# Kernel optimization log

Measured on AMD Instinct MI355X. Metric: run time of the kernel, lower is better.

Reference implementation:

```python
import jax, jax.numpy as jnp
import numpy as np

EC = 32
N = 500000
DIV_EPS = 1e-8
NO_PENALTY_THRESH = 0.005

def _rotation_matrices(rpy):
    # rpy: [EC,3] roll-pitch-yaw -> [EC,3,3]
    c = jnp.cos(rpy); s = jnp.sin(rpy)
    cx, cy, cz = c[:, 0], c[:, 1], c[:, 2]
    sx, sy, sz = s[:, 0], s[:, 1], s[:, 2]
    R = jnp.stack([
        cz * cy, cz * sy * sx - sz * cx, cz * sy * cx + sz * sx,
        sz * cy, sz * sy * sx + cz * cx, sz * sy * cx - cz * sx,
        -sy,     cy * sx,                cy * cx,
    ], axis=-1)
    return R.reshape(rpy.shape[:-1] + (3, 3))

def _eval_rbf(samples, centers, radii, rotations):
    # samples [N,3], centers/radii/rotations [EC,3] -> [EC,N]
    d = 1.0 / (radii + DIV_EPS)                      # inverse diag covariances
    R = _rotation_matrices(rotations)                # [EC,3,3]
    inv_cov = jnp.einsum('eij,ej,ekj->eik', R, d, R) # R diag(d) R^T, symmetric
    diff = samples[None, :, :] - centers[:, None, :] # [EC,N,3]
    quad = jnp.einsum('eni,eij,enj->en', diff, inv_cov, diff)
    return jnp.exp(-0.5 * quad)

def setup_inputs() -> dict:
    key = jax.random.key(0)
    ks = jax.random.split(key, 7)
    u = lambda k, shape, lo, hi: jax.random.uniform(k, shape, jnp.float32, lo, hi)
    return {
        'world_space_points': jax.random.normal(ks[0], (N, 3), jnp.float32),
        'nerflet_activations': jax.random.normal(ks[1], (EC, N, 4), jnp.float32),
        'dists': jax.random.uniform(ks[2], (N, 1), jnp.float32),
        'constants': u(ks[3], (EC, 1), 10.0, 20.0),
        'centers': u(ks[4], (EC, 3), -0.45, 0.45),
        'radii': u(ks[5], (EC, 1), 0.05, 0.06),
        'rotations': u(ks[6], (EC, 3), -np.pi, np.pi),
    }

def reference(world_space_points, nerflet_activations, dists, constants, centers, radii, rotations):
    c = jnp.abs(constants)                            # [EC,1]
    r3 = jnp.tile(jnp.abs(radii), (1, 3))             # [EC,3]
    rbfs = _eval_rbf(world_space_points, centers, r3, rotations)[:, :, None]  # [EC,N,1]
    rbfs = rbfs * c[:, None, :]                       # scaled by |constants|
    penalty = jnp.mean(jnp.sum(jnp.abs(rbfs - NO_PENALTY_THRESH), axis=0))
    alpha = 1.0 - jnp.exp(-jax.nn.relu(nerflet_activations[..., -1:]) * dists[None])  # [EC,N,1]
    rgb = jax.nn.sigmoid(nerflet_activations[..., :3])
    na = jnp.concatenate([rgb, alpha], axis=-1)       # [EC,N,4]
    rbf_sums = jnp.sum(rbfs, axis=0, keepdims=True)   # [1,N,1]
    rbfs_norm = rbfs / (rbf_sums + 0.01)
    outputs = jnp.sum(na * rbfs_norm, axis=0)         # [N,4]
    return outputs, penalty
```

## Files before the change

kernel.cpp:

```cpp
#include <hip/hip_runtime.h>
#include <math.h>

#define EC 32
#define BLOCK 256

typedef float fvec4 __attribute__((ext_vector_type(4)));

__global__ __launch_bounds__(BLOCK) void ldif_main_kernel(
    const float* __restrict__ pts,
    const fvec4* __restrict__ act,
    const float* __restrict__ dists,
    const float* __restrict__ constants,
    const float* __restrict__ centers,
    const float* __restrict__ radii,
    const float* __restrict__ rotations,
    fvec4* __restrict__ out,
    float* __restrict__ partials,
    int n) {
    __shared__ float4 sp[EC * 3];
    __shared__ float red[BLOCK];
    int tid = threadIdx.x;
    if (tid < EC) {
        int e = tid;
        float r = fabsf(radii[e]);
        float dinv = 1.0f / (r + 1e-8f);
        float rx = rotations[3 * e + 0], ry = rotations[3 * e + 1], rz = rotations[3 * e + 2];
        float cx = cosf(rx), cy = cosf(ry), cz = cosf(rz);
        float sx = sinf(rx), sy = sinf(ry), sz = sinf(rz);
        float R00 = cz * cy, R01 = cz * sy * sx - sz * cx, R02 = cz * sy * cx + sz * sx;
        float R10 = sz * cy, R11 = sz * sy * sx + cz * cx, R12 = sz * sy * cx - cz * sx;
        float R20 = -sy,     R21 = cy * sx,                R22 = cy * cx;
        float ic00 = dinv * (R00 * R00 + R01 * R01 + R02 * R02);
        float ic11 = dinv * (R10 * R10 + R11 * R11 + R12 * R12);
        float ic22 = dinv * (R20 * R20 + R21 * R21 + R22 * R22);
        float ic01 = dinv * (R00 * R10 + R01 * R11 + R02 * R12);
        float ic02 = dinv * (R00 * R20 + R01 * R21 + R02 * R22);
        float ic12 = dinv * (R10 * R20 + R11 * R21 + R12 * R22);
        const float NH = -0.72134752044f;
        float lc = log2f(fabsf(constants[e]));
        sp[3 * e + 0] = make_float4(centers[3 * e + 0], centers[3 * e + 1], centers[3 * e + 2], lc);
        sp[3 * e + 1] = make_float4(NH * ic00, NH * ic11, NH * ic22, 2.0f * NH * ic01);
        sp[3 * e + 2] = make_float4(2.0f * NH * ic02, 2.0f * NH * ic12, 0.0f, 0.0f);
    }
    __syncthreads();

    long long i = (long long)blockIdx.x * BLOCK + tid;
    float pen = 0.0f;
    if (i < n) {
        float px = pts[3 * i + 0];
        float py = pts[3 * i + 1];
        float pz = pts[3 * i + 2];
        float dl = dists[i] * 1.44269504f;

        float s = 0.0f;
        float a0 = 0.0f, a1 = 0.0f, a2 = 0.0f, a3 = 0.0f;
#pragma unroll 8
        for (int e = 0; e < EC; ++e) {
            fvec4 a = __builtin_nontemporal_load(&act[(size_t)e * (size_t)n + (size_t)i]);
            float4 p0 = sp[3 * e + 0];
            float4 p1 = sp[3 * e + 1];
            float4 p2 = sp[3 * e + 2];
            float dx = px - p0.x, dy = py - p0.y, dz = pz - p0.z;
            float q = (p1.x * dx + p1.w * dy + p2.x * dz) * dx
                    + (p1.y * dy + p2.y * dz) * dy
                    + (p1.z * dz) * dz
                    + p0.w;
            float v = __builtin_amdgcn_exp2f(q);
            s += v;
            pen += fabsf(v - 0.005f);
            float s0 = __builtin_amdgcn_rcpf(1.0f + __builtin_amdgcn_exp2f(-1.44269504f * a.x));
            float s1 = __builtin_amdgcn_rcpf(1.0f + __builtin_amdgcn_exp2f(-1.44269504f * a.y));
            float s2 = __builtin_amdgcn_rcpf(1.0f + __builtin_amdgcn_exp2f(-1.44269504f * a.z));
            float al = 1.0f - __builtin_amdgcn_exp2f(-fmaxf(a.w, 0.0f) * dl);
            a0 += v * s0;
            a1 += v * s1;
            a2 += v * s2;
            a3 += v * al;
        }
        float rn = __builtin_amdgcn_rcpf(s + 0.01f);
        fvec4 o;
        o.x = a0 * rn; o.y = a1 * rn; o.z = a2 * rn; o.w = a3 * rn;
        __builtin_nontemporal_store(o, &out[i]);
    }

    red[tid] = pen;
    __syncthreads();
    for (int st = BLOCK / 2; st > 0; st >>= 1) {
        if (tid < st) red[tid] += red[tid + st];
        __syncthreads();
    }
    if (tid == 0) partials[blockIdx.x] = red[0];
}

__global__ __launch_bounds__(BLOCK) void ldif_reduce_kernel(
    const float* __restrict__ partials, int nparts, float* __restrict__ out, int n) {
    __shared__ double rd[BLOCK];
    int tid = threadIdx.x;
    double s = 0.0;
    for (int j = tid; j < nparts; j += BLOCK) s += (double)partials[j];
    rd[tid] = s;
    __syncthreads();
    for (int st = BLOCK / 2; st > 0; st >>= 1) {
        if (tid < st) rd[tid] += rd[tid + st];
        __syncthreads();
    }
    if (tid == 0) out[0] = (float)(rd[0] / (double)n);
}

extern "C" void kernel_launch(void* const* d_in, const int* in_sizes, int n_in,
                              void* d_out, int out_size, void* d_ws, size_t ws_size,
                              hipStream_t stream) {
    const float* pts       = (const float*)d_in[0];
    const float* act       = (const float*)d_in[1];
    const float* dists     = (const float*)d_in[2];
    const float* constants = (const float*)d_in[3];
    const float* centers   = (const float*)d_in[4];
    const float* radii     = (const float*)d_in[5];
    const float* rotations = (const float*)d_in[6];
    float* out = (float*)d_out;

    int n = in_sizes[0] / 3;
    float* partials = (float*)d_ws;

    int nblocks = (n + BLOCK - 1) / BLOCK;

    ldif_main_kernel<<<nblocks, BLOCK, 0, stream>>>(
        pts, (const fvec4*)act, dists, constants, centers, radii, rotations,
        (fvec4*)out, partials, n);
    ldif_reduce_kernel<<<1, BLOCK, 0, stream>>>(partials, nblocks, out + (size_t)4 * n, n);
}
```

Before: 51.13 us.

## Fuse penalty reduction via last-block atomic counter and process two points per thread

Removes the separate reduce kernel launch by having the last block to finish, detected through an atomic counter zeroed by a memset, perform the final penalty sum. Each thread now handles two points, which gives it more independent loads and exp work in flight and halves the number of blocks. The block reduction switches to wavefront shuffles. In exchange it adds a memset and the atomic/fence logic, and raises register pressure.

```diff
diff --git a/kernel.cpp b/kernel.cpp
--- a/kernel.cpp
+++ b/kernel.cpp
@@ -3,10 +3,11 @@
 
 #define EC 32
 #define BLOCK 256
+#define PPT 2
 
 typedef float fvec4 __attribute__((ext_vector_type(4)));
 
-__global__ __launch_bounds__(BLOCK) void ldif_main_kernel(
+__global__ __launch_bounds__(BLOCK) void ldif_fused_kernel(
     const float* __restrict__ pts,
     const fvec4* __restrict__ act,
     const float* __restrict__ dists,
@@ -15,11 +16,16 @@
     const float* __restrict__ radii,
     const float* __restrict__ rotations,
     fvec4* __restrict__ out,
+    float* __restrict__ penout,
     float* __restrict__ partials,
-    int n) {
+    unsigned int* __restrict__ counter,
+    int n, int nblocks) {
     __shared__ float4 sp[EC * 3];
-    __shared__ float red[BLOCK];
-    int tid = threadIdx.x;
+    __shared__ float sred[4];
+    __shared__ double rd[BLOCK];
+    __shared__ int sdone;
+
+    const int tid = threadIdx.x;
     if (tid < EC) {
         int e = tid;
         float r = fabsf(radii[e]);
@@ -44,67 +50,101 @@
     }
     __syncthreads();
 
-    long long i = (long long)blockIdx.x * BLOCK + tid;
+    const long long i0 = (long long)blockIdx.x * (BLOCK * PPT) + tid;
+    const long long i1 = i0 + BLOCK;
+    const bool v1 = (i1 < n);
+    const long long iq = v1 ? i1 : i0;
+
     float pen = 0.0f;
-    if (i < n) {
-        float px = pts[3 * i + 0];
-        float py = pts[3 * i + 1];
-        float pz = pts[3 * i + 2];
-        float dl = dists[i] * 1.44269504f;
+    {
+        const float LOG2E = 1.44269504f;
+        float pxp = __builtin_nontemporal_load(&pts[3 * i0 + 0]);
+        float pyp = __builtin_nontemporal_load(&pts[3 * i0 + 1]);
+        float pzp = __builtin_nontemporal_load(&pts[3 * i0 + 2]);
+        float dlp = __builtin_nontemporal_load(&dists[i0]) * LOG2E;
+        float pxq = __builtin_nontemporal_load(&pts[3 * iq + 0]);
+        float pyq = __builtin_nontemporal_load(&pts[3 * iq + 1]);
+        float pzq = __builtin_nontemporal_load(&pts[3 * iq + 2]);
+        float dlq = __builtin_nontemporal_load(&dists[iq]) * LOG2E;
 
-        float s = 0.0f;
-        float a0 = 0.0f, a1 = 0.0f, a2 = 0.0f, a3 = 0.0f;
-#pragma unroll 8
+        float sP = 0.f, p0P = 0.f, p1P = 0.f, p2P = 0.f, p3P = 0.f, penP = 0.f;
+        float sQ = 0.f, p0Q = 0.f, p1Q = 0.f, p2Q = 0.f, p3Q = 0.f, penQ = 0.f;
+#pragma unroll 4
         for (int e = 0; e < EC; ++e) {
-            fvec4 a = __builtin_nontemporal_load(&act[(size_t)e * (size_t)n + (size_t)i]);
-            float4 p0 = sp[3 * e + 0];
-            float4 p1 = sp[3 * e + 1];
-            float4 p2 = sp[3 * e + 2];
-            float dx = px - p0.x, dy = py - p0.y, dz = pz - p0.z;
-            float q = (p1.x * dx + p1.w * dy + p2.x * dz) * dx
-                    + (p1.y * dy + p2.y * dz) * dy
-                    + (p1.z * dz) * dz
-                    + p0.w;
-            float v = __builtin_amdgcn_exp2f(q);
-            s += v;
-            pen += fabsf(v - 0.005f);
-            float s0 = __builtin_amdgcn_rcpf(1.0f + __builtin_amdgcn_exp2f(-1.44269504f * a.x));
-            float s1 = __builtin_amdgcn_rcpf(1.0f + __builtin_amdgcn_exp2f(-1.44269504f * a.y));
-            float s2 = __builtin_amdgcn_rcpf(1.0f + __builtin_amdgcn_exp2f(-1.44269504f * a.z));
-            float al = 1.0f - __builtin_amdgcn_exp2f(-fmaxf(a.w, 0.0f) * dl);
-            a0 += v * s0;
-            a1 += v * s1;
-            a2 += v * s2;
-            a3 += v * al;
+            fvec4 ap = __builtin_nontemporal_load(&act[(size_t)e * (size_t)n + (size_t)i0]);
+            fvec4 aq = __builtin_nontemporal_load(&act[(size_t)e * (size_t)n + (size_t)iq]);
+            float4 c0 = sp[3 * e + 0];
+            float4 c1 = sp[3 * e + 1];
+            float4 c2 = sp[3 * e + 2];
+            {
+                float dx = pxp - c0.x, dy = pyp - c0.y, dz = pzp - c0.z;
+                float q = (c1.x * dx + c1.w * dy + c2.x * dz) * dx
+                        + (c1.y * dy + c2.y * dz) * dy
+                        + (c1.z * dz) * dz + c0.w;
+                float v = __builtin_amdgcn_exp2f(q);
+                sP += v;
+                penP += fabsf(v - 0.005f);
+                float s0 = __builtin_amdgcn_rcpf(1.0f + __builtin_amdgcn_exp2f(-LOG2E * ap.x));
+                float s1 = __builtin_amdgcn_rcpf(1.0f + __builtin_amdgcn_exp2f(-LOG2E * ap.y));
+                float s2 = __builtin_amdgcn_rcpf(1.0f + __builtin_amdgcn_exp2f(-LOG2E * ap.z));
+                float al = 1.0f - __builtin_amdgcn_exp2f(-fmaxf(ap.w, 0.0f) * dlp);
+                p0P += v * s0; p1P += v * s1; p2P += v * s2; p3P += v * al;
+            }
+            {
+                float dx = pxq - c0.x, dy = pyq - c0.y, dz = pzq - c0.z;
+                float q = (c1.x * dx + c1.w * dy + c2.x * dz) * dx
+                        + (c1.y * dy + c2.y * dz) * dy
+                        + (c1.z * dz) * dz + c0.w;
+                float v = __builtin_amdgcn_exp2f(q);
+                sQ += v;
+                penQ += fabsf(v - 0.005f);
+                float s0 = __builtin_amdgcn_rcpf(1.0f + __builtin_amdgcn_exp2f(-LOG2E * aq.x));
+                float s1 = __builtin_amdgcn_rcpf(1.0f + __builtin_amdgcn_exp2f(-LOG2E * aq.y));
+                float s2 = __builtin_amdgcn_rcpf(1.0f + __builtin_amdgcn_exp2f(-LOG2E * aq.z));
+                float al = 1.0f - __builtin_amdgcn_exp2f(-fmaxf(aq.w, 0.0f) * dlq);
+                p0Q += v * s0; p1Q += v * s1; p2Q += v * s2; p3Q += v * al;
+            }
         }
-        float rn = __builtin_amdgcn_rcpf(s + 0.01f);
-        fvec4 o;
-        o.x = a0 * rn; o.y = a1 * rn; o.z = a2 * rn; o.w = a3 * rn;
-        __builtin_nontemporal_store(o, &out[i]);
+        float rnP = __builtin_amdgcn_rcpf(sP + 0.01f);
+        fvec4 oP; oP.x = p0P * rnP; oP.y = p1P * rnP; oP.z = p2P * rnP; oP.w = p3P * rnP;
+        __builtin_nontemporal_store(oP, &out[i0]);
+        if (v1) {
+            float rnQ = __builtin_amdgcn_rcpf(sQ + 0.01f);
+            fvec4 oQ; oQ.x = p0Q * rnQ; oQ.y = p1Q * rnQ; oQ.z = p2Q * rnQ; oQ.w = p3Q * rnQ;
+            __builtin_nontemporal_store(oQ, &out[i1]);
+            pen = penP + penQ;
+        } else {
+            pen = penP;
+        }
     }
 
-    red[tid] = pen;
+    float w = pen;
+#pragma unroll
+    for (int off = 32; off >= 1; off >>= 1) w += __shfl_xor(w, off);
+    if ((tid & 63) == 0) sred[tid >> 6] = w;
     __syncthreads();
-    for (int st = BLOCK / 2; st > 0; st >>= 1) {
-        if (tid < st) red[tid] += red[tid + st];
+    if (tid == 0) {
+        float bp = ((sred[0] + sred[1]) + sred[2]) + sred[3];
+        partials[blockIdx.x] = bp;
+        __threadfence();
+        unsigned int old = atomicAdd(counter, 1u);
+        sdone = (old == (unsigned int)(nblocks - 1)) ? 1 : 0;
+    }
+    __syncthreads();
+
+    if (sdone) {
+        __threadfence();
+        const volatile float* vp = partials;
+        double s = 0.0;
+        for (int j = tid; j < nblocks; j += BLOCK) s += (double)vp[j];
+        rd[tid] = s;
         __syncthreads();
+        for (int st = BLOCK / 2; st > 0; st >>= 1) {
+            if (tid < st) rd[tid] += rd[tid + st];
+            __syncthreads();
+        }
+        if (tid == 0) *penout = (float)(rd[0] / (double)n);
     }
-    if (tid == 0) partials[blockIdx.x] = red[0];
-}
-
-__global__ __launch_bounds__(BLOCK) void ldif_reduce_kernel(
-    const float* __restrict__ partials, int nparts, float* __restrict__ out, int n) {
-    __shared__ double rd[BLOCK];
-    int tid = threadIdx.x;
-    double s = 0.0;
-    for (int j = tid; j < nparts; j += BLOCK) s += (double)partials[j];
-    rd[tid] = s;
-    __syncthreads();
-    for (int st = BLOCK / 2; st > 0; st >>= 1) {
-        if (tid < st) rd[tid] += rd[tid + st];
-        __syncthreads();
-    }
-    if (tid == 0) out[0] = (float)(rd[0] / (double)n);
 }
 
 extern "C" void kernel_launch(void* const* d_in, const int* in_sizes, int n_in,
@@ -120,12 +160,13 @@
     float* out = (float*)d_out;
 
     int n = in_sizes[0] / 3;
-    float* partials = (float*)d_ws;
+    unsigned int* counter = (unsigned int*)d_ws;
+    float* partials = (float*)((char*)d_ws + 256);
 
-    int nblocks = (n + BLOCK - 1) / BLOCK;
+    int nblocks = (n + BLOCK * PPT - 1) / (BLOCK * PPT);
 
-    ldif_main_kernel<<<nblocks, BLOCK, 0, stream>>>(
+    hipMemsetAsync(d_ws, 0, sizeof(unsigned int), stream);
+    ldif_fused_kernel<<<nblocks, BLOCK, 0, stream>>>(
         pts, (const fvec4*)act, dists, constants, centers, radii, rotations,
-        (fvec4*)out, partials, n);
-    ldif_reduce_kernel<<<1, BLOCK, 0, stream>>>(partials, nblocks, out + (size_t)4 * n, n);
+        (fvec4*)out, out + (size_t)4 * n, partials, counter, n, nblocks);
 }
```

After: 96.15 us. 1.88x slower.

## Fuse penalty reduction into main kernel via last-block atomic counter

Applied to the files above, without the earlier changes.

Removes the separate reduce kernel launch. Each block now reduces its penalty partial with wavefront shuffles instead of a shared-memory tree, and the last block to finish, detected with an atomic counter and thread fences, sums all partials in double. A hipMemsetAsync is added to reset the counter on every call, which replaces the kernel launch with a memset operation. It also adds an atomic and a fence per block.

```diff
diff --git a/kernel.cpp b/kernel.cpp
--- a/kernel.cpp
+++ b/kernel.cpp
@@ -6,7 +6,7 @@
 
 typedef float fvec4 __attribute__((ext_vector_type(4)));
 
-__global__ __launch_bounds__(BLOCK) void ldif_main_kernel(
+__global__ __launch_bounds__(BLOCK) void ldif_fused_kernel(
     const float* __restrict__ pts,
     const fvec4* __restrict__ act,
     const float* __restrict__ dists,
@@ -15,11 +15,16 @@
     const float* __restrict__ radii,
     const float* __restrict__ rotations,
     fvec4* __restrict__ out,
+    float* __restrict__ penout,
     float* __restrict__ partials,
-    int n) {
+    unsigned int* __restrict__ counter,
+    int n, int nblocks) {
     __shared__ float4 sp[EC * 3];
-    __shared__ float red[BLOCK];
-    int tid = threadIdx.x;
+    __shared__ float sred[4];
+    __shared__ double rd[BLOCK];
+    __shared__ int sdone;
+
+    const int tid = threadIdx.x;
     if (tid < EC) {
         int e = tid;
         float r = fabsf(radii[e]);
@@ -47,30 +52,30 @@
     long long i = (long long)blockIdx.x * BLOCK + tid;
     float pen = 0.0f;
     if (i < n) {
+        const float LOG2E = 1.44269504f;
         float px = pts[3 * i + 0];
         float py = pts[3 * i + 1];
         float pz = pts[3 * i + 2];
-        float dl = dists[i] * 1.44269504f;
+        float dl = dists[i] * LOG2E;
 
         float s = 0.0f;
         float a0 = 0.0f, a1 = 0.0f, a2 = 0.0f, a3 = 0.0f;
 #pragma unroll 8
         for (int e = 0; e < EC; ++e) {
             fvec4 a = __builtin_nontemporal_load(&act[(size_t)e * (size_t)n + (size_t)i]);
-            float4 p0 = sp[3 * e + 0];
-            float4 p1 = sp[3 * e + 1];
-            float4 p2 = sp[3 * e + 2];
-            float dx = px - p0.x, dy = py - p0.y, dz = pz - p0.z;
-            float q = (p1.x * dx + p1.w * dy + p2.x * dz) * dx
-                    + (p1.y * dy + p2.y * dz) * dy
-                    + (p1.z * dz) * dz
-                    + p0.w;
+            float4 c0 = sp[3 * e + 0];
+            float4 c1 = sp[3 * e + 1];
+            float4 c2 = sp[3 * e + 2];
+            float dx = px - c0.x, dy = py - c0.y, dz = pz - c0.z;
+            float q = (c1.x * dx + c1.w * dy + c2.x * dz) * dx
+                    + (c1.y * dy + c2.y * dz) * dy
+                    + (c1.z * dz) * dz + c0.w;
             float v = __builtin_amdgcn_exp2f(q);
             s += v;
             pen += fabsf(v - 0.005f);
-            float s0 = __builtin_amdgcn_rcpf(1.0f + __builtin_amdgcn_exp2f(-1.44269504f * a.x));
-            float s1 = __builtin_amdgcn_rcpf(1.0f + __builtin_amdgcn_exp2f(-1.44269504f * a.y));
-            float s2 = __builtin_amdgcn_rcpf(1.0f + __builtin_amdgcn_exp2f(-1.44269504f * a.z));
+            float s0 = __builtin_amdgcn_rcpf(1.0f + __builtin_amdgcn_exp2f(-LOG2E * a.x));
+            float s1 = __builtin_amdgcn_rcpf(1.0f + __builtin_amdgcn_exp2f(-LOG2E * a.y));
+            float s2 = __builtin_amdgcn_rcpf(1.0f + __builtin_amdgcn_exp2f(-LOG2E * a.z));
             float al = 1.0f - __builtin_amdgcn_exp2f(-fmaxf(a.w, 0.0f) * dl);
             a0 += v * s0;
             a1 += v * s1;
@@ -83,28 +88,33 @@
         __builtin_nontemporal_store(o, &out[i]);
     }
 
-    red[tid] = pen;
+    float w = pen;
+#pragma unroll
+    for (int off = 32; off >= 1; off >>= 1) w += __shfl_xor(w, off);
+    if ((tid & 63) == 0) sred[tid >> 6] = w;
     __syncthreads();
-    for (int st = BLOCK / 2; st > 0; st >>= 1) {
-        if (tid < st) red[tid] += red[tid + st];
+    if (tid == 0) {
+        float bp = ((sred[0] + sred[1]) + sred[2]) + sred[3];
+        partials[blockIdx.x] = bp;
+        __threadfence();
+        unsigned int old = atomicAdd(counter, 1u);
+        sdone = (old == (unsigned int)(nblocks - 1)) ? 1 : 0;
+    }
+    __syncthreads();
+
+    if (sdone) {
+        __threadfence();
+        const volatile float* vp = partials;
+        double s = 0.0;
+        for (int j = tid; j < nblocks; j += BLOCK) s += (double)vp[j];
+        rd[tid] = s;
         __syncthreads();
+        for (int st = BLOCK / 2; st > 0; st >>= 1) {
+            if (tid < st) rd[tid] += rd[tid + st];
+            __syncthreads();
+        }
+        if (tid == 0) *penout = (float)(rd[0] / (double)n);
     }
-    if (tid == 0) partials[blockIdx.x] = red[0];
-}
-
-__global__ __launch_bounds__(BLOCK) void ldif_reduce_kernel(
-    const float* __restrict__ partials, int nparts, float* __restrict__ out, int n) {
-    __shared__ double rd[BLOCK];
-    int tid = threadIdx.x;
-    double s = 0.0;
-    for (int j = tid; j < nparts; j += BLOCK) s += (double)partials[j];
-    rd[tid] = s;
-    __syncthreads();
-    for (int st = BLOCK / 2; st > 0; st >>= 1) {
-        if (tid < st) rd[tid] += rd[tid + st];
-        __syncthreads();
-    }
-    if (tid == 0) out[0] = (float)(rd[0] / (double)n);
 }
 
 extern "C" void kernel_launch(void* const* d_in, const int* in_sizes, int n_in,
@@ -120,12 +130,13 @@
     float* out = (float*)d_out;
 
     int n = in_sizes[0] / 3;
-    float* partials = (float*)d_ws;
+    unsigned int* counter = (unsigned int*)d_ws;
+    float* partials = (float*)((char*)d_ws + 256);
 
     int nblocks = (n + BLOCK - 1) / BLOCK;
 
-    ldif_main_kernel<<<nblocks, BLOCK, 0, stream>>>(
+    hipMemsetAsync(d_ws, 0, sizeof(unsigned int), stream);
+    ldif_fused_kernel<<<nblocks, BLOCK, 0, stream>>>(
         pts, (const fvec4*)act, dists, constants, centers, radii, rotations,
-        (fvec4*)out, partials, n);
-    ldif_reduce_kernel<<<1, BLOCK, 0, stream>>>(partials, nblocks, out + (size_t)4 * n, n);
+        (fvec4*)out, out + (size_t)4 * n, partials, counter, n, nblocks);
 }
```

Result: slower. 140.2 us (+174.3%).
